# Optimization experiments

Measured on AMD Instinct MI355X. Metric: run time of the kernel, lower is better.

The kernel has to match this reference:

```python
import jax, jax.numpy as jnp
import numpy as np

B, T, D = 32, 4096, 64
K = 512
COMMITMENT_COST = 0.25


def setup_inputs() -> dict:
    key = jax.random.key(0)
    kz, kw = jax.random.split(key)
    z = jax.random.normal(kz, (B, T, D), dtype=jnp.float32)
    # matches nn.init.uniform_(weight, -1/K, 1/K)
    W = jax.random.uniform(kw, (K, D), dtype=jnp.float32, minval=-1.0 / K, maxval=1.0 / K)
    return {"z": z, "W": W}


def reference(z, W):
    b, t, d = z.shape
    z_flat = z.reshape(-1, d)                                   # [N, D]
    # squared euclidean distances via ||z||^2 + ||w||^2 - 2 z.w
    dist = (jnp.sum(z_flat * z_flat, axis=1, keepdims=True)
            + jnp.sum(W * W, axis=1)
            - 2.0 * z_flat @ W.T)                               # [N, K]
    indices = jnp.argmin(dist, axis=1)                          # [N]
    z_q = W[indices].reshape(b, t, d)                           # gather
    # straight-through estimator
    z_q_st = z + jax.lax.stop_gradient(z_q - z)
    loss = COMMITMENT_COST * jnp.mean((z - jax.lax.stop_gradient(z_q_st)) ** 2)
    return z_q_st, indices.reshape(b, t), loss
```

## Files before the change

### kernel.cpp

```cpp
#include <hip/hip_runtime.h>
#include <hip/hip_bf16.h>
#include <math.h>

#define NROWS 131072
#define KC    512
#define DD    64
#define NELEM (NROWS * DD)

#define OUT_IDX_OFF  NELEM
#define OUT_LOSS_OFF (NELEM + NROWS)

#define MARGIN 3e-5f

#define WSO_CNT   0
#define WSO_LOSS  8
#define WSO_WNORM 64
#define WSO_BH    4096
#define WSO_BL    (WSO_BH + 65536)
#define WSO_LIST  (WSO_BL + 65536)

typedef __attribute__((ext_vector_type(8))) short short8;
typedef __attribute__((ext_vector_type(4))) float f32x4;

__device__ __forceinline__ short f2bf_bits(float f) {
  __hip_bfloat16 h = __float2bfloat16(f);
  short s; __builtin_memcpy(&s, &h, 2); return s;
}
__device__ __forceinline__ float bfbits2f(short s) {
  __hip_bfloat16 h; __builtin_memcpy(&h, &s, 2);
  return __bfloat162float(h);
}
__device__ __forceinline__ void cvt8(const float* __restrict__ p, short8& hi, short8& lo) {
#pragma unroll
  for (int j = 0; j < 8; j++) {
    float f = p[j];
    short hb = f2bf_bits(f);
    float r = f - bfbits2f(hb);
    hi[j] = hb;
    lo[j] = f2bf_bits(r);
  }
}

__device__ __forceinline__ float np_sumsq64(const float* __restrict__ p) {
#pragma clang fp contract(off)
  float r0 = p[0] * p[0], r1 = p[1] * p[1], r2 = p[2] * p[2], r3 = p[3] * p[3];
  float r4 = p[4] * p[4], r5 = p[5] * p[5], r6 = p[6] * p[6], r7 = p[7] * p[7];
  for (int i = 8; i < 64; i += 8) {
    r0 = r0 + p[i + 0] * p[i + 0];
    r1 = r1 + p[i + 1] * p[i + 1];
    r2 = r2 + p[i + 2] * p[i + 2];
    r3 = r3 + p[i + 3] * p[i + 3];
    r4 = r4 + p[i + 4] * p[i + 4];
    r5 = r5 + p[i + 5] * p[i + 5];
    r6 = r6 + p[i + 6] * p[i + 6];
    r7 = r7 + p[i + 7] * p[i + 7];
  }
  return ((r0 + r1) + (r2 + r3)) + ((r4 + r5) + (r6 + r7));
}

__global__ void k_prep(const float* __restrict__ W, short8* __restrict__ Bh,
                       short8* __restrict__ Bl, float* __restrict__ wnorm) {
  int gtid = blockIdx.x * blockDim.x + threadIdx.x;
  int t = gtid >> 7, rem = gtid & 127;
  int h = rem >> 6, L = rem & 63;
  int cw = (t << 4) + (L & 15);
  int dbase = (h << 5) + ((L >> 4) << 3);
  short8 hi, lo;
  cvt8(W + (cw << 6) + dbase, hi, lo);
  Bh[gtid] = hi;
  Bl[gtid] = lo;
  if (gtid < KC) wnorm[gtid] = np_sumsq64(W + (gtid << 6));
}

__global__ __launch_bounds__(256) void k_screen(
    const float* __restrict__ z, const float* __restrict__ W,
    const short8* __restrict__ Bh, const short8* __restrict__ Bl,
    const float* __restrict__ wnorm, float* __restrict__ out,
    int* __restrict__ flagList, int* __restrict__ flagCnt,
    float* __restrict__ lossSum) {
  const int lane = threadIdx.x & 63;
  const int wave = threadIdx.x >> 6;
  const int rowBase = blockIdx.x * 256 + wave * 64;
  const int m = lane & 15, quad = lane >> 4;

  short8 Ah[4][2], Al[4][2];
#pragma unroll
  for (int mt = 0; mt < 4; mt++) {
    const float* zp = z + (size_t)(rowBase + (mt << 4) + m) * DD + (quad << 3);
#pragma unroll
    for (int h = 0; h < 2; h++) cvt8(zp + (h << 5), Ah[mt][h], Al[mt][h]);
  }

  float b1[4][4], b2[4][4];
  int bi[4][4];
#pragma unroll
  for (int mt = 0; mt < 4; mt++)
#pragma unroll
    for (int r = 0; r < 4; r++) { b1[mt][r] = 1e30f; b2[mt][r] = 1e30f; bi[mt][r] = 0; }

  for (int t = 0; t < 32; t++) {
    short8 Bhf[2], Blf[2];
#pragma unroll
    for (int h = 0; h < 2; h++) {
      Bhf[h] = Bh[((t * 2 + h) << 6) + lane];
      Blf[h] = Bl[((t * 2 + h) << 6) + lane];
    }
    float wn = wnorm[(t << 4) + m];

    f32x4 acc[4] = {{0.f, 0.f, 0.f, 0.f}, {0.f, 0.f, 0.f, 0.f},
                    {0.f, 0.f, 0.f, 0.f}, {0.f, 0.f, 0.f, 0.f}};
#pragma unroll
    for (int h = 0; h < 2; h++) {
#pragma unroll
      for (int mt = 0; mt < 4; mt++)
        acc[mt] = __builtin_amdgcn_mfma_f32_16x16x32_bf16(Ah[mt][h], Bhf[h], acc[mt], 0, 0, 0);
#pragma unroll
      for (int mt = 0; mt < 4; mt++)
        acc[mt] = __builtin_amdgcn_mfma_f32_16x16x32_bf16(Al[mt][h], Bhf[h], acc[mt], 0, 0, 0);
#pragma unroll
      for (int mt = 0; mt < 4; mt++)
        acc[mt] = __builtin_amdgcn_mfma_f32_16x16x32_bf16(Ah[mt][h], Blf[h], acc[mt], 0, 0, 0);
    }

    int colv = (t << 4) + m;
#pragma unroll
    for (int mt = 0; mt < 4; mt++)
#pragma unroll
      for (int r = 0; r < 4; r++) {
        float s = fmaf(-2.0f, acc[mt][r], wn);
        if (s < b1[mt][r]) { b2[mt][r] = b1[mt][r]; b1[mt][r] = s; bi[mt][r] = colv; }
        else b2[mt][r] = fminf(b2[mt][r], s);
      }
  }

#pragma unroll
  for (int off = 1; off < 16; off <<= 1) {
#pragma unroll
    for (int mt = 0; mt < 4; mt++)
#pragma unroll
      for (int r = 0; r < 4; r++) {
        float o1 = __shfl_xor(b1[mt][r], off, 64);
        float o2 = __shfl_xor(b2[mt][r], off, 64);
        int oi = __shfl_xor(bi[mt][r], off, 64);
        if (o1 < b1[mt][r] || (o1 == b1[mt][r] && oi < bi[mt][r])) {
          b2[mt][r] = fminf(b1[mt][r], o2);
          b1[mt][r] = o1; bi[mt][r] = oi;
        } else {
          b2[mt][r] = fminf(b2[mt][r], o1);
        }
      }
  }

  float lossAcc = 0.f;
#pragma unroll
  for (int mt = 0; mt < 4; mt++)
#pragma unroll
    for (int lr = 0; lr < 16; lr++) {
      const int q = lr >> 2, r = lr & 3;
      int ki = __shfl(bi[mt][r], q << 4, 64);
      float b1r = __shfl(b1[mt][r], q << 4, 64);
      float b2r = __shfl(b2[mt][r], q << 4, 64);
      int row = rowBase + (mt << 4) + lr;
      float zv = z[(size_t)row * DD + lane];
      float w = W[(ki << 6) + lane];
      float tt = w - zv;
      float o = zv + tt;
      out[(size_t)row * DD + lane] = o;
      float dl = zv - o;
      lossAcc = fmaf(dl, dl, lossAcc);
      if (lane == 0) {
        out[OUT_IDX_OFF + row] = (float)ki;
        if (b2r - b1r < MARGIN) {
          int slot = atomicAdd(flagCnt, 1);
          flagList[slot] = row;
        }
      }
    }

#pragma unroll
  for (int off = 1; off < 64; off <<= 1) lossAcc += __shfl_xor(lossAcc, off, 64);
  if (lane == 0) atomicAdd(lossSum, lossAcc);
}

__global__ void k_refine(const float* __restrict__ z, const float* __restrict__ W,
                         const float* __restrict__ wnp, float* __restrict__ out,
                         const int* __restrict__ flagList,
                         const int* __restrict__ flagCnt,
                         float* __restrict__ lossSum) {
  int nflag = *flagCnt;
  int lane = threadIdx.x & 63;
  int wave = (blockIdx.x * blockDim.x + threadIdx.x) >> 6;
  int nWaves = (gridDim.x * blockDim.x) >> 6;

  for (int f = wave; f < nflag; f += nWaves) {
    int row = flagList[f];
    const float* zr = z + (size_t)row * DD;
    float A = np_sumsq64(zr);

    float best = 1e30f;
    int bk = 0x7fffffff;
#pragma unroll
    for (int j = 0; j < KC / 64; j++) {
      int k = lane + (j << 6);
      const float* wk = W + (k << 6);
      double cd = 0.0;
      for (int d = 0; d < DD; d++) cd = fma((double)zr[d], (double)wk[d], cd);
      float twoC = (float)(2.0 * cd);
      float dist;
      {
#pragma clang fp contract(off)
        float t1 = A + wnp[k];
        dist = t1 - twoC;
      }
      if (dist < best || (dist == best && k < bk)) { best = dist; bk = k; }
    }
#pragma unroll
    for (int off = 1; off < 64; off <<= 1) {
      float ov = __shfl_xor(best, off, 64);
      int ok = __shfl_xor(bk, off, 64);
      if (ov < best || (ov == best && ok < bk)) { best = ov; bk = ok; }
    }

    int kold = (int)out[OUT_IDX_OFF + row];
    if (bk != kold) {
      float zv = zr[lane];
      float wN = W[(bk << 6) + lane];
      float oOld = out[(size_t)row * DD + lane];
      float tN = wN - zv;
      float oN = zv + tN;
      out[(size_t)row * DD + lane] = oN;
      float dN = zv - oN, dO = zv - oOld;
      float delta = dN * dN - dO * dO;
#pragma unroll
      for (int off = 1; off < 64; off <<= 1) delta += __shfl_xor(delta, off, 64);
      if (lane == 0) {
        atomicAdd(lossSum, delta);
        out[OUT_IDX_OFF + row] = (float)bk;
      }
    }
  }
}

__global__ void k_finalize(const float* __restrict__ lossSum, float* __restrict__ out) {
  out[OUT_LOSS_OFF] = 0.25f * (*lossSum) / (float)NELEM;
}

extern "C" void kernel_launch(void* const* d_in, const int* in_sizes, int n_in,
                              void* d_out, int out_size, void* d_ws, size_t ws_size,
                              hipStream_t stream) {
  const float* z = (const float*)d_in[0];
  const float* W = (const float*)d_in[1];
  float* out = (float*)d_out;
  char* ws = (char*)d_ws;

  int* flagCnt = (int*)(ws + WSO_CNT);
  float* lossSum = (float*)(ws + WSO_LOSS);
  float* wnorm = (float*)(ws + WSO_WNORM);
  short8* Bh = (short8*)(ws + WSO_BH);
  short8* Bl = (short8*)(ws + WSO_BL);
  int* flagList = (int*)(ws + WSO_LIST);

  hipMemsetAsync(d_ws, 0, 64, stream);

  k_prep<<<16, 256, 0, stream>>>(W, Bh, Bl, wnorm);
  k_screen<<<NROWS / 256, 256, 0, stream>>>(z, W, Bh, Bl, wnorm, out,
                                            flagList, flagCnt, lossSum);
  k_refine<<<256, 256, 0, stream>>>(z, W, wnorm, out, flagList, flagCnt, lossSum);
  k_finalize<<<1, 1, 0, stream>>>(lossSum, out);
}
```

Measured before the change: 190.7 us.

## Halve rows per wave, prefetch codebook fragments, vectorize epilogue, fuse finalize

Reduces each wave's row tile from 64 to 32 rows (MT=2) and adds launch bounds so more waves can be resident. The next codebook tile's B fragments are software-prefetched into registers to hide load latency. The epilogue now uses the MFMA output layout directly, with float4 loads and stores instead of per-row shuffles. The memset and finalize launches are folded into the prep kernel and a last-block-done counter in refine. In exchange, each wave reuses B fragments across fewer rows and the grid is twice as large.

New measurement: 202.8 us. 1.06x slower.

```diff
diff --git a/kernel.cpp b/kernel.cpp
--- a/kernel.cpp
+++ b/kernel.cpp
@@ -13,6 +13,7 @@
 #define MARGIN 3e-5f
 
 #define WSO_CNT   0
+#define WSO_DONE  4
 #define WSO_LOSS  8
 #define WSO_WNORM 64
 #define WSO_BH    4096
@@ -59,8 +60,11 @@
 }
 
 __global__ void k_prep(const float* __restrict__ W, short8* __restrict__ Bh,
-                       short8* __restrict__ Bl, float* __restrict__ wnorm) {
+                       short8* __restrict__ Bl, float* __restrict__ wnorm,
+                       int* __restrict__ flagCnt, int* __restrict__ doneCnt,
+                       float* __restrict__ lossSum) {
   int gtid = blockIdx.x * blockDim.x + threadIdx.x;
+  if (gtid == 0) { *flagCnt = 0; *doneCnt = 0; *lossSum = 0.0f; }
   int t = gtid >> 7, rem = gtid & 127;
   int h = rem >> 6, L = rem & 63;
   int cw = (t << 4) + (L & 15);
@@ -72,7 +76,11 @@
   if (gtid < KC) wnorm[gtid] = np_sumsq64(W + (gtid << 6));
 }
 
-__global__ __launch_bounds__(256) void k_screen(
+#define MT 2
+#define ROWS_PER_WAVE (MT * 16)
+#define ROWS_PER_BLOCK (ROWS_PER_WAVE * 4)
+
+__global__ __launch_bounds__(256, 4) void k_screen(
     const float* __restrict__ z, const float* __restrict__ W,
     const short8* __restrict__ Bh, const short8* __restrict__ Bl,
     const float* __restrict__ wnorm, float* __restrict__ out,
@@ -80,63 +88,75 @@
     float* __restrict__ lossSum) {
   const int lane = threadIdx.x & 63;
   const int wave = threadIdx.x >> 6;
-  const int rowBase = blockIdx.x * 256 + wave * 64;
+  const int rowBase = blockIdx.x * ROWS_PER_BLOCK + wave * ROWS_PER_WAVE;
   const int m = lane & 15, quad = lane >> 4;
 
-  short8 Ah[4][2], Al[4][2];
-#pragma unroll
-  for (int mt = 0; mt < 4; mt++) {
+  short8 Ah[MT][2], Al[MT][2];
+#pragma unroll
+  for (int mt = 0; mt < MT; mt++) {
     const float* zp = z + (size_t)(rowBase + (mt << 4) + m) * DD + (quad << 3);
 #pragma unroll
     for (int h = 0; h < 2; h++) cvt8(zp + (h << 5), Ah[mt][h], Al[mt][h]);
   }
 
-  float b1[4][4], b2[4][4];
-  int bi[4][4];
-#pragma unroll
-  for (int mt = 0; mt < 4; mt++)
+  float b1[MT][4], b2[MT][4];
+  int bi[MT][4];
+#pragma unroll
+  for (int mt = 0; mt < MT; mt++)
 #pragma unroll
     for (int r = 0; r < 4; r++) { b1[mt][r] = 1e30f; b2[mt][r] = 1e30f; bi[mt][r] = 0; }
 
+  short8 cBh[2], cBl[2];
+#pragma unroll
+  for (int h = 0; h < 2; h++) {
+    cBh[h] = Bh[(h << 6) + lane];
+    cBl[h] = Bl[(h << 6) + lane];
+  }
+  float cwn = wnorm[m];
+
   for (int t = 0; t < 32; t++) {
-    short8 Bhf[2], Blf[2];
+    const int tn = (t + 1) & 31;
+    short8 nBh[2], nBl[2];
 #pragma unroll
     for (int h = 0; h < 2; h++) {
-      Bhf[h] = Bh[((t * 2 + h) << 6) + lane];
-      Blf[h] = Bl[((t * 2 + h) << 6) + lane];
-    }
-    float wn = wnorm[(t << 4) + m];
-
-    f32x4 acc[4] = {{0.f, 0.f, 0.f, 0.f}, {0.f, 0.f, 0.f, 0.f},
-                    {0.f, 0.f, 0.f, 0.f}, {0.f, 0.f, 0.f, 0.f}};
+      nBh[h] = Bh[(((tn << 1) + h) << 6) + lane];
+      nBl[h] = Bl[(((tn << 1) + h) << 6) + lane];
+    }
+    float nwn = wnorm[(tn << 4) + m];
+
+    f32x4 acc[MT] = {{0.f, 0.f, 0.f, 0.f}, {0.f, 0.f, 0.f, 0.f}};
 #pragma unroll
     for (int h = 0; h < 2; h++) {
 #pragma unroll
-      for (int mt = 0; mt < 4; mt++)
-        acc[mt] = __builtin_amdgcn_mfma_f32_16x16x32_bf16(Ah[mt][h], Bhf[h], acc[mt], 0, 0, 0);
-#pragma unroll
-      for (int mt = 0; mt < 4; mt++)
-        acc[mt] = __builtin_amdgcn_mfma_f32_16x16x32_bf16(Al[mt][h], Bhf[h], acc[mt], 0, 0, 0);
-#pragma unroll
-      for (int mt = 0; mt < 4; mt++)
-        acc[mt] = __builtin_amdgcn_mfma_f32_16x16x32_bf16(Ah[mt][h], Blf[h], acc[mt], 0, 0, 0);
+      for (int mt = 0; mt < MT; mt++)
+        acc[mt] = __builtin_amdgcn_mfma_f32_16x16x32_bf16(Ah[mt][h], cBh[h], acc[mt], 0, 0, 0);
+#pragma unroll
+      for (int mt = 0; mt < MT; mt++)
+        acc[mt] = __builtin_amdgcn_mfma_f32_16x16x32_bf16(Al[mt][h], cBh[h], acc[mt], 0, 0, 0);
+#pragma unroll
+      for (int mt = 0; mt < MT; mt++)
+        acc[mt] = __builtin_amdgcn_mfma_f32_16x16x32_bf16(Ah[mt][h], cBl[h], acc[mt], 0, 0, 0);
     }
 
     int colv = (t << 4) + m;
 #pragma unroll
-    for (int mt = 0; mt < 4; mt++)
+    for (int mt = 0; mt < MT; mt++)
 #pragma unroll
       for (int r = 0; r < 4; r++) {
-        float s = fmaf(-2.0f, acc[mt][r], wn);
+        float s = fmaf(-2.0f, acc[mt][r], cwn);
         if (s < b1[mt][r]) { b2[mt][r] = b1[mt][r]; b1[mt][r] = s; bi[mt][r] = colv; }
         else b2[mt][r] = fminf(b2[mt][r], s);
       }
+
+    cBh[0] = nBh[0]; cBh[1] = nBh[1];
+    cBl[0] = nBl[0]; cBl[1] = nBl[1];
+    cwn = nwn;
   }
 
 #pragma unroll
   for (int off = 1; off < 16; off <<= 1) {
 #pragma unroll
-    for (int mt = 0; mt < 4; mt++)
+    for (int mt = 0; mt < MT; mt++)
 #pragma unroll
       for (int r = 0; r < 4; r++) {
         float o1 = __shfl_xor(b1[mt][r], off, 64);
@@ -153,24 +173,25 @@
 
   float lossAcc = 0.f;
 #pragma unroll
-  for (int mt = 0; mt < 4; mt++)
-#pragma unroll
-    for (int lr = 0; lr < 16; lr++) {
-      const int q = lr >> 2, r = lr & 3;
-      int ki = __shfl(bi[mt][r], q << 4, 64);
-      float b1r = __shfl(b1[mt][r], q << 4, 64);
-      float b2r = __shfl(b2[mt][r], q << 4, 64);
-      int row = rowBase + (mt << 4) + lr;
-      float zv = z[(size_t)row * DD + lane];
-      float w = W[(ki << 6) + lane];
-      float tt = w - zv;
-      float o = zv + tt;
-      out[(size_t)row * DD + lane] = o;
-      float dl = zv - o;
-      lossAcc = fmaf(dl, dl, lossAcc);
-      if (lane == 0) {
+  for (int mt = 0; mt < MT; mt++)
+#pragma unroll
+    for (int r = 0; r < 4; r++) {
+      const int row = rowBase + (mt << 4) + (quad << 2) + r;
+      const int ki = bi[mt][r];
+      f32x4 zv = *(const f32x4*)(z + (size_t)row * DD + (m << 2));
+      f32x4 wv = *(const f32x4*)(W + (ki << 6) + (m << 2));
+      f32x4 ov;
+#pragma unroll
+      for (int j = 0; j < 4; j++) {
+        float tt = wv[j] - zv[j];
+        ov[j] = zv[j] + tt;
+        float dl = zv[j] - ov[j];
+        lossAcc = fmaf(dl, dl, lossAcc);
+      }
+      *(f32x4*)(out + (size_t)row * DD + (m << 2)) = ov;
+      if (m == 0) {
         out[OUT_IDX_OFF + row] = (float)ki;
-        if (b2r - b1r < MARGIN) {
+        if (b2[mt][r] - b1[mt][r] < MARGIN) {
           int slot = atomicAdd(flagCnt, 1);
           flagList[slot] = row;
         }
@@ -186,7 +207,7 @@
                          const float* __restrict__ wnp, float* __restrict__ out,
                          const int* __restrict__ flagList,
                          const int* __restrict__ flagCnt,
-                         float* __restrict__ lossSum) {
+                         float* __restrict__ lossSum, int* __restrict__ doneCnt) {
   int nflag = *flagCnt;
   int lane = threadIdx.x & 63;
   int wave = (blockIdx.x * blockDim.x + threadIdx.x) >> 6;
@@ -239,10 +260,16 @@
       }
     }
   }
-}
-
-__global__ void k_finalize(const float* __restrict__ lossSum, float* __restrict__ out) {
-  out[OUT_LOSS_OFF] = 0.25f * (*lossSum) / (float)NELEM;
+
+  __syncthreads();
+  if (threadIdx.x == 0) {
+    __threadfence();
+    int d = atomicAdd(doneCnt, 1);
+    if (d == (int)gridDim.x - 1) {
+      float s = atomicAdd(lossSum, 0.0f);
+      out[OUT_LOSS_OFF] = 0.25f * s / (float)NELEM;
+    }
+  }
 }
 
 extern "C" void kernel_launch(void* const* d_in, const int* in_sizes, int n_in,
@@ -254,17 +281,16 @@
   char* ws = (char*)d_ws;
 
   int* flagCnt = (int*)(ws + WSO_CNT);
+  int* doneCnt = (int*)(ws + WSO_DONE);
   float* lossSum = (float*)(ws + WSO_LOSS);
   float* wnorm = (float*)(ws + WSO_WNORM);
   short8* Bh = (short8*)(ws + WSO_BH);
   short8* Bl = (short8*)(ws + WSO_BL);
   int* flagList = (int*)(ws + WSO_LIST);
 
-  hipMemsetAsync(d_ws, 0, 64, stream);
-
-  k_prep<<<16, 256, 0, stream>>>(W, Bh, Bl, wnorm);
-  k_screen<<<NROWS / 256, 256, 0, stream>>>(z, W, Bh, Bl, wnorm, out,
-                                            flagList, flagCnt, lossSum);
-  k_refine<<<256, 256, 0, stream>>>(z, W, wnorm, out, flagList, flagCnt, lossSum);
-  k_finalize<<<1, 1, 0, stream>>>(lossSum, out);
-}
+  k_prep<<<16, 256, 0, stream>>>(W, Bh, Bl, wnorm, flagCnt, doneCnt, lossSum);
+  k_screen<<<NROWS / ROWS_PER_BLOCK, 256, 0, stream>>>(z, W, Bh, Bl, wnorm, out,
+                                                       flagList, flagCnt, lossSum);
+  k_refine<<<256, 256, 0, stream>>>(z, W, wnorm, out, flagList, flagCnt,
+                                    lossSum, doneCnt);
+}
```

## Fold memset and finalize into kernels, transpose codebook for coalesced refine reads

Applied to the files above, without the earlier changes.

The workspace memset moves into k_prep and the separate finalize kernel is dropped. The last refine block to finish, detected with a done counter and atomics, now writes the loss, which cuts two launches from the stream. k_prep also writes a transposed copy of W so that the lanes in refine's fp64 dot-product loop read consecutive addresses. The flag list is capped to a fixed size, which could silently skip refinement if more rows than the cap get flagged.

After: 217.2 us. 13.9% more time.

```diff
diff --git a/kernel.cpp b/kernel.cpp
--- a/kernel.cpp
+++ b/kernel.cpp
@@ -13,11 +13,14 @@
 #define MARGIN 3e-5f
 
 #define WSO_CNT   0
+#define WSO_DONE  4
 #define WSO_LOSS  8
 #define WSO_WNORM 64
 #define WSO_BH    4096
 #define WSO_BL    (WSO_BH + 65536)
-#define WSO_LIST  (WSO_BL + 65536)
+#define WSO_WT    (WSO_BL + 65536)
+#define WSO_LIST  (WSO_WT + 131072)
+#define FLAG_CAP  32768
 
 typedef __attribute__((ext_vector_type(8))) short short8;
 typedef __attribute__((ext_vector_type(4))) float f32x4;
@@ -59,17 +62,28 @@
 }
 
 __global__ void k_prep(const float* __restrict__ W, short8* __restrict__ Bh,
-                       short8* __restrict__ Bl, float* __restrict__ wnorm) {
+                       short8* __restrict__ Bl, float* __restrict__ wnorm,
+                       float* __restrict__ Wt, int* __restrict__ flagCnt,
+                       int* __restrict__ doneCnt, float* __restrict__ lossSum) {
   int gtid = blockIdx.x * blockDim.x + threadIdx.x;
-  int t = gtid >> 7, rem = gtid & 127;
-  int h = rem >> 6, L = rem & 63;
-  int cw = (t << 4) + (L & 15);
-  int dbase = (h << 5) + ((L >> 4) << 3);
-  short8 hi, lo;
-  cvt8(W + (cw << 6) + dbase, hi, lo);
-  Bh[gtid] = hi;
-  Bl[gtid] = lo;
-  if (gtid < KC) wnorm[gtid] = np_sumsq64(W + (gtid << 6));
+  if (gtid == 0) { *flagCnt = 0; *doneCnt = 0; *lossSum = 0.0f; }
+
+  {
+    int k = gtid >> 6, d = gtid & 63;
+    Wt[(d << 9) + k] = W[(k << 6) + d];
+  }
+
+  if (gtid < 4096) {
+    int t = gtid >> 7, rem = gtid & 127;
+    int h = rem >> 6, L = rem & 63;
+    int cw = (t << 4) + (L & 15);
+    int dbase = (h << 5) + ((L >> 4) << 3);
+    short8 hi, lo;
+    cvt8(W + (cw << 6) + dbase, hi, lo);
+    Bh[gtid] = hi;
+    Bl[gtid] = lo;
+    if (gtid < KC) wnorm[gtid] = np_sumsq64(W + (gtid << 6));
+  }
 }
 
 __global__ __launch_bounds__(256) void k_screen(
@@ -172,7 +186,7 @@
         out[OUT_IDX_OFF + row] = (float)ki;
         if (b2r - b1r < MARGIN) {
           int slot = atomicAdd(flagCnt, 1);
-          flagList[slot] = row;
+          if (slot < FLAG_CAP) flagList[slot] = row;
         }
       }
     }
@@ -183,11 +197,13 @@
 }
 
 __global__ void k_refine(const float* __restrict__ z, const float* __restrict__ W,
-                         const float* __restrict__ wnp, float* __restrict__ out,
+                         const float* __restrict__ Wt, const float* __restrict__ wnp,
+                         float* __restrict__ out,
                          const int* __restrict__ flagList,
                          const int* __restrict__ flagCnt,
-                         float* __restrict__ lossSum) {
+                         float* __restrict__ lossSum, int* __restrict__ doneCnt) {
   int nflag = *flagCnt;
+  if (nflag > FLAG_CAP) nflag = FLAG_CAP;
   int lane = threadIdx.x & 63;
   int wave = (blockIdx.x * blockDim.x + threadIdx.x) >> 6;
   int nWaves = (gridDim.x * blockDim.x) >> 6;
@@ -202,9 +218,9 @@
 #pragma unroll
     for (int j = 0; j < KC / 64; j++) {
       int k = lane + (j << 6);
-      const float* wk = W + (k << 6);
       double cd = 0.0;
-      for (int d = 0; d < DD; d++) cd = fma((double)zr[d], (double)wk[d], cd);
+      for (int d = 0; d < DD; d++)
+        cd = fma((double)zr[d], (double)Wt[(d << 9) + k], cd);
       float twoC = (float)(2.0 * cd);
       float dist;
       {
@@ -239,10 +255,16 @@
       }
     }
   }
-}
-
-__global__ void k_finalize(const float* __restrict__ lossSum, float* __restrict__ out) {
-  out[OUT_LOSS_OFF] = 0.25f * (*lossSum) / (float)NELEM;
+
+  __syncthreads();
+  if (threadIdx.x == 0) {
+    __threadfence();
+    int d = atomicAdd(doneCnt, 1);
+    if (d == (int)gridDim.x - 1) {
+      float s = atomicAdd(lossSum, 0.0f);
+      out[OUT_LOSS_OFF] = 0.25f * s / (float)NELEM;
+    }
+  }
 }
 
 extern "C" void kernel_launch(void* const* d_in, const int* in_sizes, int n_in,
@@ -254,17 +276,17 @@
   char* ws = (char*)d_ws;
 
   int* flagCnt = (int*)(ws + WSO_CNT);
+  int* doneCnt = (int*)(ws + WSO_DONE);
   float* lossSum = (float*)(ws + WSO_LOSS);
   float* wnorm = (float*)(ws + WSO_WNORM);
   short8* Bh = (short8*)(ws + WSO_BH);
   short8* Bl = (short8*)(ws + WSO_BL);
+  float* Wt = (float*)(ws + WSO_WT);
   int* flagList = (int*)(ws + WSO_LIST);
 
-  hipMemsetAsync(d_ws, 0, 64, stream);
-
-  k_prep<<<16, 256, 0, stream>>>(W, Bh, Bl, wnorm);
+  k_prep<<<128, 256, 0, stream>>>(W, Bh, Bl, wnorm, Wt, flagCnt, doneCnt, lossSum);
   k_screen<<<NROWS / 256, 256, 0, stream>>>(z, W, Bh, Bl, wnorm, out,
                                             flagList, flagCnt, lossSum);
-  k_refine<<<256, 256, 0, stream>>>(z, W, wnorm, out, flagList, flagCnt, lossSum);
-  k_finalize<<<1, 1, 0, stream>>>(lossSum, out);
-}
+  k_refine<<<256, 256, 0, stream>>>(z, W, Wt, wnorm, out, flagList, flagCnt,
+                                    lossSum, doneCnt);
+}
```
